# Performance work log

Hardware: AMD Instinct MI355X
Metric: run time of the kernel (lower is better)

The kernel has to match this reference:

```python
import jax, jax.numpy as jnp
import numpy as np

GRID = 16
K = 2
NW = (GRID - K + 1) ** 2  # 225 sliding 2x2 windows on the 16x16 grid


def _make_mask():
    idx = np.arange(GRID * GRID).reshape(GRID, GRID)
    wins = np.stack([idx[i:i + K, j:j + K].ravel()
                     for i in range(GRID - K + 1) for j in range(GRID - K + 1)])
    m = np.zeros((NW, GRID * GRID), np.float32)
    m[np.arange(NW)[:, None], wins] = 1.0
    return jnp.asarray(m)

MASK = _make_mask()          # [225, 256] window -> covered cells
MASK_COUNT = MASK.sum(0)     # windows covering each cell
BN_SCALE = np.float32(1.0 / np.sqrt(1.0 + 1e-5))  # eval BN, running mean=0 var=1


def _adapter(x, w1, w2):
    return jax.nn.relu(jax.nn.relu(x @ w1.T) @ w2.T)


def _bn(x, g, b):
    return x * (g * BN_SCALE) + b


def _head(x, w1, b1, g2, be2, w2, b2, g3, be3, w3, b3):
    x = _bn(jax.nn.relu(x @ w1.T + b1), g2, be2)
    x = _bn(jax.nn.relu(x @ w2.T + b2), g3, be3)
    return jax.nn.sigmoid(x @ w3.T + b3)[:, 0]


def setup_inputs() -> dict:
    B, L, P, D, R, S = 64, 3, 225, 640, 1800, 240
    key = jax.random.key(0)
    ks = jax.random.split(key, 16)
    n = lambda k, s, sc=1.0: jax.random.normal(k, s, jnp.float32) * sc
    te = n(ks[3], (2, D)); te = te / jnp.linalg.norm(te, axis=-1, keepdims=True)
    pr = n(ks[5], (L, R, D)); pr = pr / jnp.linalg.norm(pr, axis=-1, keepdims=True)
    w = 0.05
    return dict(
        image=n(ks[0], (B, 3, S, S)),
        image_embeds=n(ks[1], (B, D)),
        patch_embeds=n(ks[2], (L, B, P, D)),
        text_embeds=te,
        image_embeds_ref=n(ks[4], (1, D)),
        patch_embeds_ref=pr,
        a_w1=n(ks[6], (160, D), w), a_w2=n(ks[7], (D, 160), w),
        r_w1=n(ks[8], (128, D), w), r_b1=jnp.zeros((128,)),
        r_g2=jnp.ones((128,)), r_be2=jnp.zeros((128,)),
        r_w2=n(ks[9], (64, 128), w), r_b2=jnp.zeros((64,)),
        r_g3=jnp.ones((64,)), r_be3=jnp.zeros((64,)),
        r_w3=n(ks[10], (1, 64), w), r_b3=jnp.zeros((1,)),
        h_w1=n(ks[11], (128, P), w), h_b1=jnp.zeros((128,)),
        h_g2=jnp.ones((128,)), h_be2=jnp.zeros((128,)),
        h_w2=n(ks[12], (64, 128), w), h_b2=jnp.zeros((64,)),
        h_g3=jnp.ones((64,)), h_be3=jnp.zeros((64,)),
        h_w3=n(ks[13], (1, 64), w), h_b3=jnp.zeros((1,)),
    )


def reference(image, image_embeds, patch_embeds, text_embeds, image_embeds_ref,
              patch_embeds_ref, a_w1, a_w2,
              r_w1, r_b1, r_g2, r_be2, r_w2, r_b2, r_g3, r_be3, r_w3, r_b3,
              h_w1, h_b1, h_g2, h_be2, h_w2, h_b2, h_g3, h_be3, h_w3, h_b3):
    pe = patch_embeds / jnp.linalg.norm(patch_embeds, axis=-1, keepdims=True)
    nie = image_embeds / jnp.linalg.norm(image_embeds, axis=-1, keepdims=True)
    text_score = jax.nn.softmax(100.0 * nie @ text_embeds.T, axis=-1)[:, 1]
    # kNN-style min-distance over reference patches: [L,B,P,R]
    sim = jnp.einsum('lbpd,lrd->lbpr', pe, patch_embeds_ref)
    patch_ref_map = ((1.0 - sim).min(axis=3) / 2.0).mean(axis=0)  # [B,P]
    fg_score = patch_ref_map.max(axis=1)
    diff = image_embeds_ref - _adapter(image_embeds, a_w1, a_w2)
    img_ref_score = _head(diff, r_w1, r_b1, r_g2, r_be2, r_w2, r_b2, r_g3, r_be3, r_w3, r_b3)
    holistic = (text_score + img_ref_score)[:, None] + patch_ref_map  # [B,225]
    hl_score = _head(holistic, h_w1, h_b1, h_g2, h_be2, h_w2, h_b2, h_g3, h_be3, h_w3, h_b3)
    final_score = (hl_score + fg_score) / 2.0
    # harmonic aggregation of window scores onto the 16x16 grid
    heat = (MASK_COUNT / ((1.0 / holistic) @ MASK)).reshape(-1, GRID, GRID)
    hmap = jax.image.resize(heat, (heat.shape[0], image.shape[2], image.shape[3]), 'bilinear')
    return final_score, hmap
```

## Files before the change

### kernel.cpp

```cpp
#include <hip/hip_runtime.h>
#include <stdint.h>
#include <math.h>

#define L_DIM 3
#define B_DIM 64
#define P_DIM 225
#define D_DIM 640
#define R_DIM 1800
#define S_DIM 240
#define M_TOT 14400
#define M_PAD 14464
#define N_PAD 2048
#define MT 113
#define NT 8
#define KT 20
#define BNSCALE 0.99999500003749981f

typedef __bf16 bf16x8 __attribute__((ext_vector_type(8)));
typedef float f32x4 __attribute__((ext_vector_type(4)));

__device__ __forceinline__ unsigned short f2bf(float f) {
    union { float f; unsigned u; } v; v.f = f;
    unsigned u = v.u;
    unsigned r = (u + 0x7FFFu + ((u >> 16) & 1u)) >> 16;
    return (unsigned short)r;
}

__global__ __launch_bounds__(256)
void k_convert(const float* __restrict__ pe, const float* __restrict__ per,
               unsigned short* __restrict__ abf, unsigned short* __restrict__ rbf,
               float* __restrict__ rnorm)
{
    const int AROWS = L_DIM * M_PAD;
    int wid = (blockIdx.x * 256 + threadIdx.x) >> 6;
    int lane = threadIdx.x & 63;
    const ushort4 z4 = {0, 0, 0, 0};
    if (wid < AROWS) {
        int l = wid / M_PAD, r = wid - l * M_PAD;
        unsigned short* dst = abf + (size_t)wid * D_DIM;
        if (r < M_TOT) {
            const float4* src = (const float4*)(pe + ((size_t)l * M_TOT + r) * D_DIM);
            float ss = 0.f;
            #pragma unroll
            for (int it = 0; it < 3; ++it) {
                int idx = it * 64 + lane;
                if (idx < 160) {
                    float4 v = src[idx];
                    ss += v.x * v.x + v.y * v.y + v.z * v.z + v.w * v.w;
                    ushort4 o;
                    o.x = f2bf(v.x); o.y = f2bf(v.y); o.z = f2bf(v.z); o.w = f2bf(v.w);
                    *(ushort4*)(dst + idx * 4) = o;
                }
            }
            #pragma unroll
            for (int m = 32; m; m >>= 1) ss += __shfl_xor(ss, m);
            if (lane == 0) rnorm[l * M_TOT + r] = rsqrtf(ss);
        } else {
            #pragma unroll
            for (int it = 0; it < 3; ++it) {
                int idx = it * 64 + lane;
                if (idx < 160) *(ushort4*)(dst + idx * 4) = z4;
            }
        }
    } else {
        int w2 = wid - AROWS;
        int l = w2 / N_PAD, r = w2 - l * N_PAD;
        unsigned short* dst = rbf + (size_t)w2 * D_DIM;
        if (r < R_DIM) {
            const float4* src = (const float4*)(per + ((size_t)l * R_DIM + r) * D_DIM);
            #pragma unroll
            for (int it = 0; it < 3; ++it) {
                int idx = it * 64 + lane;
                if (idx < 160) {
                    float4 v = src[idx];
                    ushort4 o;
                    o.x = f2bf(v.x); o.y = f2bf(v.y); o.z = f2bf(v.z); o.w = f2bf(v.w);
                    *(ushort4*)(dst + idx * 4) = o;
                }
            }
        } else {
            #pragma unroll
            for (int it = 0; it < 3; ++it) {
                int idx = it * 64 + lane;
                if (idx < 160) *(ushort4*)(dst + idx * 4) = z4;
            }
        }
    }
}

#define MFMA(A, B, C) __builtin_amdgcn_mfma_f32_16x16x32_bf16((A), (B), (C), 0, 0, 0)
#define GLL(SRC, DSTOFF)                                                     \
    __builtin_amdgcn_global_load_lds(                                        \
        (const __attribute__((address_space(1))) void*)(SRC),               \
        (__attribute__((address_space(3))) void*)(lds + (DSTOFF)), 16, 0, 0)

__global__ __launch_bounds__(512, 4)
void k_gemm_max(const unsigned short* __restrict__ abf,
                const unsigned short* __restrict__ rbf,
                float* __restrict__ pmax)
{
    __shared__ unsigned short lds[36864];
    __shared__ float red[4][128];

    int bid = blockIdx.x;
    int v = (bid & 7) * 339 + (bid >> 3);
    int l = v / (MT * NT);
    int rem = v - l * (MT * NT);
    int mt = rem >> 3;
    int nt = rem & 7;

    int tid = threadIdx.x;
    int wid = tid >> 6, lane = tid & 63;
    int wm = wid >> 2;
    int wn = wid & 3;
    int lane15 = lane & 15, lg = lane >> 4;

    int lpr = lane >> 3;
    int c2  = (lane & 7) ^ lpr;
    int kc  = c2 & 3;
    int rsub = lpr * 2 + (c2 >> 2);
    const unsigned short* gA = abf + (size_t)(l * M_PAD + mt * 128) * D_DIM;
    const unsigned short* gB = rbf + (size_t)(l * N_PAD + nt * 256) * D_DIM;
    const unsigned short* pA  = gA + (size_t)(wid * 16 + rsub) * D_DIM + kc * 8;
    const unsigned short* pB0 = gB + (size_t)(wid * 16 + rsub) * D_DIM + kc * 8;
    const unsigned short* pB1 = gB + (size_t)(wid * 16 + 128 + rsub) * D_DIM + kc * 8;

    int pcom = (((lane15 & 1) << 2) + lg) ^ ((lane15 >> 1) & 7);
    int aoff = (wm * 32 + (lane15 >> 1)) * 64 + pcom * 8;
    int boff = (wn * 32 + (lane15 >> 1)) * 64 + pcom * 8;

    f32x4 acc[4][4];
    #pragma unroll
    for (int mi = 0; mi < 4; ++mi)
        #pragma unroll
        for (int nj = 0; nj < 4; ++nj)
            acc[mi][nj] = f32x4{0.f, 0.f, 0.f, 0.f};

    GLL(pA, wid * 512);
    GLL(pB0, 12288 + wid * 512);
    GLL(pB1, 12288 + (8 + wid) * 512);
    GLL(pA + 32, 4096 + wid * 512);
    GLL(pB0 + 32, 12288 + 8192 + wid * 512);
    GLL(pB1 + 32, 12288 + 8192 + (8 + wid) * 512);
    asm volatile("s_waitcnt vmcnt(3)" ::: "memory");
    __builtin_amdgcn_s_barrier();

    int cur = 0;
    for (int t = 0; t < KT; ++t) {
        int wr = cur + 2; if (wr >= 3) wr -= 3;
        int aB = cur * 4096;
        int bB = 12288 + cur * 8192;

        bf16x8 a[4], b[4];
        #pragma unroll
        for (int mi = 0; mi < 4; ++mi)
            a[mi] = *(const bf16x8*)(lds + aB + aoff + mi * 512);
        #pragma unroll
        for (int nj = 0; nj < 4; ++nj)
            b[nj] = *(const bf16x8*)(lds + bB + boff + nj * 512);

        int koff = (t + 2 < KT ? t + 2 : KT - 1) * 32;
        GLL(pA + koff, wr * 4096 + wid * 512);
        GLL(pB0 + koff, 12288 + wr * 8192 + wid * 512);
        GLL(pB1 + koff, 12288 + wr * 8192 + (8 + wid) * 512);
        asm volatile("s_waitcnt vmcnt(3)" ::: "memory");
        __builtin_amdgcn_s_barrier();

        __builtin_amdgcn_s_setprio(1);
        #pragma unroll
        for (int mi = 0; mi < 4; ++mi)
            #pragma unroll
            for (int nj = 0; nj < 4; ++nj)
                acc[mi][nj] = MFMA(a[mi], b[nj], acc[mi][nj]);
        __builtin_amdgcn_s_setprio(0);

        cur = (cur == 2) ? 0 : cur + 1;
    }

    __syncthreads();

    int colbase = nt * 256 + wn * 64 + lane15;
    #pragma unroll
    for (int mi = 0; mi < 4; ++mi) {
        float t[4] = {-__builtin_inff(), -__builtin_inff(),
                      -__builtin_inff(), -__builtin_inff()};
        #pragma unroll
        for (int nj = 0; nj < 4; ++nj) {
            if (colbase + nj * 16 < R_DIM) {
                #pragma unroll
                for (int r = 0; r < 4; ++r) t[r] = fmaxf(t[r], acc[mi][nj][r]);
            }
        }
        #pragma unroll
        for (int m = 1; m <= 8; m <<= 1) {
            #pragma unroll
            for (int r = 0; r < 4; ++r) t[r] = fmaxf(t[r], __shfl_xor(t[r], m));
        }
        if (lane15 == 0) {
            int rb = wm * 64 + mi * 16 + lg * 4;
            #pragma unroll
            for (int r = 0; r < 4; ++r) red[wn][rb + r] = t[r];
        }
    }
    __syncthreads();
    if (tid < 128) {
        float vmx = fmaxf(fmaxf(red[0][tid], red[1][tid]),
                          fmaxf(red[2][tid], red[3][tid]));
        pmax[((size_t)l * NT + nt) * M_PAD + mt * 128 + tid] = vmx;
    }
}

__device__ __forceinline__ float block_sum8(float v, volatile float* scratch) {
    #pragma unroll
    for (int m = 32; m; m >>= 1) v += __shfl_xor(v, m);
    int w = threadIdx.x >> 6;
    __syncthreads();
    if ((threadIdx.x & 63) == 0) scratch[w] = v;
    __syncthreads();
    float r = 0.f;
    #pragma unroll
    for (int i = 0; i < 8; ++i) r += scratch[i];
    return r;
}
__device__ __forceinline__ float block_max8(float v, volatile float* scratch) {
    #pragma unroll
    for (int m = 32; m; m >>= 1) v = fmaxf(v, __shfl_xor(v, m));
    int w = threadIdx.x >> 6;
    __syncthreads();
    if ((threadIdx.x & 63) == 0) scratch[w] = v;
    __syncthreads();
    float r = scratch[0];
    #pragma unroll
    for (int i = 1; i < 8; ++i) r = fmaxf(r, scratch[i]);
    return r;
}

__global__ __launch_bounds__(512)
void k_small(const float* __restrict__ ie, const float* __restrict__ te,
             const float* __restrict__ ier,
             const float* __restrict__ a_w1, const float* __restrict__ a_w2,
             const float* __restrict__ r_w1, const float* __restrict__ r_b1,
             const float* __restrict__ r_g2, const float* __restrict__ r_be2,
             const float* __restrict__ r_w2, const float* __restrict__ r_b2,
             const float* __restrict__ r_g3, const float* __restrict__ r_be3,
             const float* __restrict__ r_w3, const float* __restrict__ r_b3,
             const float* __restrict__ h_w1, const float* __restrict__ h_b1,
             const float* __restrict__ h_g2, const float* __restrict__ h_be2,
             const float* __restrict__ h_w2, const float* __restrict__ h_b2,
             const float* __restrict__ h_g3, const float* __restrict__ h_be3,
             const float* __restrict__ h_w3, const float* __restrict__ h_b3,
             const float* __restrict__ pmax, const float* __restrict__ rnorm,
             float* __restrict__ out_score, float* __restrict__ outh)
{
    int b = blockIdx.x, tid = threadIdx.x;
    __shared__ float x[D_DIM];
    __shared__ float h1[160];
    __shared__ float dif[D_DIM];
    __shared__ float z1[128];
    __shared__ float z2[64];
    __shared__ float hol[P_DIM];
    __shared__ float rcp[P_DIM];
    __shared__ float heatl[256];
    __shared__ float scratch[8];

    for (int i = tid; i < D_DIM; i += 512) x[i] = ie[b * D_DIM + i];
    __syncthreads();

    float ss = 0.f, d0 = 0.f, d1 = 0.f;
    for (int i = tid; i < D_DIM; i += 512) {
        float v = x[i];
        ss += v * v;
        d0 += v * te[i];
        d1 += v * te[D_DIM + i];
    }
    float ssum = block_sum8(ss, scratch);
    float dd0 = block_sum8(d0, scratch);
    float dd1 = block_sum8(d1, scratch);
    float tscore = 1.f / (1.f + expf(100.f * rsqrtf(ssum) * (dd0 - dd1)));

    for (int o = tid; o < 160; o += 512) {
        const float* w = a_w1 + (size_t)o * D_DIM;
        float s0 = 0, s1 = 0, s2 = 0, s3 = 0;
        for (int d = 0; d < D_DIM; d += 4) {
            s0 += x[d] * w[d]; s1 += x[d + 1] * w[d + 1];
            s2 += x[d + 2] * w[d + 2]; s3 += x[d + 3] * w[d + 3];
        }
        h1[o] = fmaxf((s0 + s1) + (s2 + s3), 0.f);
    }
    __syncthreads();
    for (int d = tid; d < D_DIM; d += 512) {
        const float* w = a_w2 + (size_t)d * 160;
        float s0 = 0, s1 = 0, s2 = 0, s3 = 0;
        for (int o = 0; o < 160; o += 4) {
            s0 += h1[o] * w[o]; s1 += h1[o + 1] * w[o + 1];
            s2 += h1[o + 2] * w[o + 2]; s3 += h1[o + 3] * w[o + 3];
        }
        dif[d] = ier[d] - fmaxf((s0 + s1) + (s2 + s3), 0.f);
    }
    __syncthreads();

    for (int o = tid; o < 128; o += 512) {
        const float* w = r_w1 + (size_t)o * D_DIM;
        float s0 = 0, s1 = 0, s2 = 0, s3 = 0;
        for (int d = 0; d < D_DIM; d += 4) {
            s0 += dif[d] * w[d]; s1 += dif[d + 1] * w[d + 1];
            s2 += dif[d + 2] * w[d + 2]; s3 += dif[d + 3] * w[d + 3];
        }
        float s = (s0 + s1) + (s2 + s3) + r_b1[o];
        z1[o] = fmaxf(s, 0.f) * (r_g2[o] * BNSCALE) + r_be2[o];
    }
    __syncthreads();
    for (int o = tid; o < 64; o += 512) {
        const float* w = r_w2 + (size_t)o * 128;
        float s = r_b2[o];
        for (int d = 0; d < 128; ++d) s += z1[d] * w[d];
        z2[o] = fmaxf(s, 0.f) * (r_g3[o] * BNSCALE) + r_be3[o];
    }
    __syncthreads();
    float sp = (tid < 64) ? z2[tid] * r_w3[tid] : 0.f;
    float irs = 1.f / (1.f + expf(-(block_sum8(sp, scratch) + r_b3[0])));

    float fgp = -__builtin_inff();
    float base = tscore + irs;
    for (int p = tid; p < P_DIM; p += 512) {
        int r = b * P_DIM + p;
        float s = 0.f;
        #pragma unroll
        for (int l = 0; l < L_DIM; ++l) {
            float m = -__builtin_inff();
            #pragma unroll
            for (int t = 0; t < NT; ++t)
                m = fmaxf(m, pmax[((size_t)l * NT + t) * M_PAD + r]);
            s += m * rnorm[l * M_TOT + r];
        }
        float pv = (3.0f - s) / 6.0f;
        fgp = fmaxf(fgp, pv);
        float h = base + pv;
        hol[p] = h;
        rcp[p] = 1.f / h;
    }
    float fg = block_max8(fgp, scratch);

    for (int o = tid; o < 128; o += 512) {
        const float* w = h_w1 + (size_t)o * P_DIM;
        float s = h_b1[o];
        for (int d = 0; d < P_DIM; ++d) s += hol[d] * w[d];
        z1[o] = fmaxf(s, 0.f) * (h_g2[o] * BNSCALE) + h_be2[o];
    }
    __syncthreads();
    for (int o = tid; o < 64; o += 512) {
        const float* w = h_w2 + (size_t)o * 128;
        float s = h_b2[o];
        for (int d = 0; d < 128; ++d) s += z1[d] * w[d];
        z2[o] = fmaxf(s, 0.f) * (h_g3[o] * BNSCALE) + h_be3[o];
    }
    __syncthreads();
    float sp2 = (tid < 64) ? z2[tid] * h_w3[tid] : 0.f;
    float hl_in = block_sum8(sp2, scratch) + h_b3[0];
    if (tid == 0) {
        float hl = 1.f / (1.f + expf(-hl_in));
        out_score[b] = (hl + fg) * 0.5f;
    }

    if (tid < 256) {
        int r = tid >> 4, c = tid & 15;
        float s = 0.f, cnt = 0.f;
        #pragma unroll
        for (int di = -1; di <= 0; ++di) {
            int i = r + di;
            if (i < 0 || i > 14) continue;
            #pragma unroll
            for (int dj = -1; dj <= 0; ++dj) {
                int j = c + dj;
                if (j < 0 || j > 14) continue;
                s += rcp[i * 15 + j];
                cnt += 1.f;
            }
        }
        heatl[tid] = cnt / s;
    }
    __syncthreads();

    float* dst = outh + (size_t)b * (S_DIM * S_DIM);
    for (int px = tid; px < S_DIM * S_DIM; px += 512) {
        int y = px / S_DIM, xc = px - y * S_DIM;
        float sy = fminf(fmaxf((y - 7) * (1.0f / 15.0f), 0.f), 15.f);
        float sx = fminf(fmaxf((xc - 7) * (1.0f / 15.0f), 0.f), 15.f);
        int y0 = (int)sy, x0 = (int)sx;
        int y1 = min(y0 + 1, 15), x1 = min(x0 + 1, 15);
        float fy = sy - (float)y0, fx = sx - (float)x0;
        float v00 = heatl[y0 * 16 + x0], v01 = heatl[y0 * 16 + x1];
        float v10 = heatl[y1 * 16 + x0], v11 = heatl[y1 * 16 + x1];
        float vv = (1.f - fy) * ((1.f - fx) * v00 + fx * v01)
                 + fy * ((1.f - fx) * v10 + fx * v11);
        dst[px] = vv;
    }
}

extern "C" void kernel_launch(void* const* d_in, const int* in_sizes, int n_in,
                              void* d_out, int out_size, void* d_ws, size_t ws_size,
                              hipStream_t stream)
{
    (void)in_sizes; (void)n_in; (void)out_size; (void)ws_size;
    const float* image_embeds = (const float*)d_in[1];
    const float* patch_embeds = (const float*)d_in[2];
    const float* text_embeds  = (const float*)d_in[3];
    const float* ier          = (const float*)d_in[4];
    const float* per          = (const float*)d_in[5];
    const float* a_w1 = (const float*)d_in[6];
    const float* a_w2 = (const float*)d_in[7];
    const float* r_w1 = (const float*)d_in[8];
    const float* r_b1 = (const float*)d_in[9];
    const float* r_g2 = (const float*)d_in[10];
    const float* r_be2 = (const float*)d_in[11];
    const float* r_w2 = (const float*)d_in[12];
    const float* r_b2 = (const float*)d_in[13];
    const float* r_g3 = (const float*)d_in[14];
    const float* r_be3 = (const float*)d_in[15];
    const float* r_w3 = (const float*)d_in[16];
    const float* r_b3 = (const float*)d_in[17];
    const float* h_w1 = (const float*)d_in[18];
    const float* h_b1 = (const float*)d_in[19];
    const float* h_g2 = (const float*)d_in[20];
    const float* h_be2 = (const float*)d_in[21];
    const float* h_w2 = (const float*)d_in[22];
    const float* h_b2 = (const float*)d_in[23];
    const float* h_g3 = (const float*)d_in[24];
    const float* h_be3 = (const float*)d_in[25];
    const float* h_w3 = (const float*)d_in[26];
    const float* h_b3 = (const float*)d_in[27];

    char* ws = (char*)d_ws;
    size_t off = 0;
    auto take = [&](size_t bytes) -> void* {
        void* p = ws + off;
        off += (bytes + 255) & ~(size_t)255;
        return p;
    };
    float* rnorm = (float*)take((size_t)L_DIM * M_TOT * 4);
    float* pmax  = (float*)take((size_t)L_DIM * NT * M_PAD * 4);
    unsigned short* abf = (unsigned short*)take((size_t)L_DIM * M_PAD * D_DIM * 2);
    unsigned short* rbf = (unsigned short*)take((size_t)L_DIM * N_PAD * D_DIM * 2);

    float* out_f = (float*)d_out;

    k_convert<<<dim3((L_DIM * M_PAD + L_DIM * N_PAD) / 4), dim3(256), 0, stream>>>(
        patch_embeds, per, abf, rbf, rnorm);
    k_gemm_max<<<dim3(L_DIM * MT * NT), dim3(512), 0, stream>>>(abf, rbf, pmax);
    k_small<<<dim3(B_DIM), dim3(512), 0, stream>>>(image_embeds, text_embeds, ier,
        a_w1, a_w2, r_w1, r_b1, r_g2, r_be2, r_w2, r_b2, r_g3, r_be3, r_w3, r_b3,
        h_w1, h_b1, h_g2, h_be2, h_w2, h_b2, h_g3, h_be3, h_w3, h_b3,
        pmax, rnorm, out_f, out_f + B_DIM);
}
```

Baseline: 221.8 us.

## Reshape GEMM-max tile to 256x128 with BK=64 double-buffered LDS pipeline

```diff
diff --git a/kernel.cpp b/kernel.cpp
--- a/kernel.cpp
+++ b/kernel.cpp
@@ -9,11 +9,11 @@
 #define R_DIM 1800
 #define S_DIM 240
 #define M_TOT 14400
-#define M_PAD 14464
-#define N_PAD 2048
-#define MT 113
-#define NT 8
-#define KT 20
+#define M_PAD 14592
+#define N_PAD 1920
+#define MT 57
+#define NT 15
+#define KT 10
 #define BNSCALE 0.99999500003749981f
 
 typedef __bf16 bf16x8 __attribute__((ext_vector_type(8)));
@@ -94,40 +94,43 @@
         (const __attribute__((address_space(1))) void*)(SRC),               \
         (__attribute__((address_space(3))) void*)(lds + (DSTOFF)), 16, 0, 0)
 
-__global__ __launch_bounds__(512, 4)
+__global__ __launch_bounds__(512, 1)
 void k_gemm_max(const unsigned short* __restrict__ abf,
                 const unsigned short* __restrict__ rbf,
                 float* __restrict__ pmax)
 {
-    __shared__ unsigned short lds[36864];
-    __shared__ float red[4][128];
+    __shared__ unsigned short lds[49152];
+    __shared__ float red[2][256];
 
     int bid = blockIdx.x;
-    int v = (bid & 7) * 339 + (bid >> 3);
+    int xcd = bid & 7, idx = bid >> 3;
+    int v = (xcd < 5 ? xcd * 321 : 5 * 321 + (xcd - 5) * 320) + idx;
     int l = v / (MT * NT);
     int rem = v - l * (MT * NT);
-    int mt = rem >> 3;
-    int nt = rem & 7;
+    int mt = rem / NT;
+    int nt = rem - mt * NT;
 
     int tid = threadIdx.x;
     int wid = tid >> 6, lane = tid & 63;
-    int wm = wid >> 2;
-    int wn = wid & 3;
+    int wm = wid >> 1;
+    int wn = wid & 1;
     int lane15 = lane & 15, lg = lane >> 4;
-
-    int lpr = lane >> 3;
-    int c2  = (lane & 7) ^ lpr;
-    int kc  = c2 & 3;
-    int rsub = lpr * 2 + (c2 >> 2);
-    const unsigned short* gA = abf + (size_t)(l * M_PAD + mt * 128) * D_DIM;
-    const unsigned short* gB = rbf + (size_t)(l * N_PAD + nt * 256) * D_DIM;
-    const unsigned short* pA  = gA + (size_t)(wid * 16 + rsub) * D_DIM + kc * 8;
-    const unsigned short* pB0 = gB + (size_t)(wid * 16 + rsub) * D_DIM + kc * 8;
-    const unsigned short* pB1 = gB + (size_t)(wid * 16 + 128 + rsub) * D_DIM + kc * 8;
-
-    int pcom = (((lane15 & 1) << 2) + lg) ^ ((lane15 >> 1) & 7);
-    int aoff = (wm * 32 + (lane15 >> 1)) * 64 + pcom * 8;
-    int boff = (wn * 32 + (lane15 >> 1)) * 64 + pcom * 8;
+    int sA = lane15 & 7;
+    int sw0 = (lg ^ sA) << 3;
+    int sw1 = ((4 + lg) ^ sA) << 3;
+    int arow0 = wm * 64 + lane15;
+    int brow0 = wn * 64 + lane15;
+
+    int rowc = lane >> 3;
+    int scol = ((lane & 7) ^ rowc) << 3;
+    const unsigned short* gA = abf + (size_t)(l * M_PAD + mt * 256) * D_DIM;
+    const unsigned short* gB = rbf + (size_t)(l * N_PAD + nt * 128) * D_DIM;
+    const unsigned short* pA0 = gA + (size_t)(wid * 8 + rowc) * D_DIM + scol;
+    const unsigned short* pA1 = gA + (size_t)(64 + wid * 8 + rowc) * D_DIM + scol;
+    const unsigned short* pA2 = gA + (size_t)(128 + wid * 8 + rowc) * D_DIM + scol;
+    const unsigned short* pA3 = gA + (size_t)(192 + wid * 8 + rowc) * D_DIM + scol;
+    const unsigned short* pB0 = gB + (size_t)(wid * 8 + rowc) * D_DIM + scol;
+    const unsigned short* pB1 = gB + (size_t)(64 + wid * 8 + rowc) * D_DIM + scol;
 
     f32x4 acc[4][4];
     #pragma unroll
@@ -136,50 +139,61 @@
         for (int nj = 0; nj < 4; ++nj)
             acc[mi][nj] = f32x4{0.f, 0.f, 0.f, 0.f};
 
-    GLL(pA, wid * 512);
-    GLL(pB0, 12288 + wid * 512);
-    GLL(pB1, 12288 + (8 + wid) * 512);
-    GLL(pA + 32, 4096 + wid * 512);
-    GLL(pB0 + 32, 12288 + 8192 + wid * 512);
-    GLL(pB1 + 32, 12288 + 8192 + (8 + wid) * 512);
-    asm volatile("s_waitcnt vmcnt(3)" ::: "memory");
-    __builtin_amdgcn_s_barrier();
-
-    int cur = 0;
+    GLL(pA0, wid * 512);
+    GLL(pA1, (8 + wid) * 512);
+    GLL(pA2, (16 + wid) * 512);
+    GLL(pA3, (24 + wid) * 512);
+    GLL(pB0, 32768 + wid * 512);
+    GLL(pB1, 32768 + (8 + wid) * 512);
+
+    int buf = 0;
     for (int t = 0; t < KT; ++t) {
-        int wr = cur + 2; if (wr >= 3) wr -= 3;
-        int aB = cur * 4096;
-        int bB = 12288 + cur * 8192;
-
-        bf16x8 a[4], b[4];
-        #pragma unroll
-        for (int mi = 0; mi < 4; ++mi)
-            a[mi] = *(const bf16x8*)(lds + aB + aoff + mi * 512);
-        #pragma unroll
-        for (int nj = 0; nj < 4; ++nj)
-            b[nj] = *(const bf16x8*)(lds + bB + boff + nj * 512);
-
-        int koff = (t + 2 < KT ? t + 2 : KT - 1) * 32;
-        GLL(pA + koff, wr * 4096 + wid * 512);
-        GLL(pB0 + koff, 12288 + wr * 8192 + wid * 512);
-        GLL(pB1 + koff, 12288 + wr * 8192 + (8 + wid) * 512);
-        asm volatile("s_waitcnt vmcnt(3)" ::: "memory");
+        int aB = buf * 16384;
+        int bB = 32768 + buf * 8192;
+
+        asm volatile("s_waitcnt vmcnt(0)" ::: "memory");
         __builtin_amdgcn_s_barrier();
 
+        bf16x8 a[4][2], b[4][2];
+        #pragma unroll
+        for (int mi = 0; mi < 4; ++mi) {
+            a[mi][0] = *(const bf16x8*)(lds + aB + (arow0 + mi * 16) * 64 + sw0);
+            a[mi][1] = *(const bf16x8*)(lds + aB + (arow0 + mi * 16) * 64 + sw1);
+        }
+        #pragma unroll
+        for (int nj = 0; nj < 4; ++nj) {
+            b[nj][0] = *(const bf16x8*)(lds + bB + (brow0 + nj * 16) * 64 + sw0);
+            b[nj][1] = *(const bf16x8*)(lds + bB + (brow0 + nj * 16) * 64 + sw1);
+        }
+
+        if (t + 1 < KT) {
+            int ko = (t + 1) * 64;
+            int oaB = (buf ^ 1) * 16384;
+            int obB = 32768 + (buf ^ 1) * 8192;
+            GLL(pA0 + ko, oaB + wid * 512);
+            GLL(pA1 + ko, oaB + (8 + wid) * 512);
+            GLL(pA2 + ko, oaB + (16 + wid) * 512);
+            GLL(pA3 + ko, oaB + (24 + wid) * 512);
+            GLL(pB0 + ko, obB + wid * 512);
+            GLL(pB1 + ko, obB + (8 + wid) * 512);
+        }
+
         __builtin_amdgcn_s_setprio(1);
         #pragma unroll
-        for (int mi = 0; mi < 4; ++mi)
-            #pragma unroll
-            for (int nj = 0; nj < 4; ++nj)
-                acc[mi][nj] = MFMA(a[mi], b[nj], acc[mi][nj]);
+        for (int ks = 0; ks < 2; ++ks)
+            #pragma unroll
+            for (int mi = 0; mi < 4; ++mi)
+                #pragma unroll
+                for (int nj = 0; nj < 4; ++nj)
+                    acc[mi][nj] = MFMA(a[mi][ks], b[nj][ks], acc[mi][nj]);
         __builtin_amdgcn_s_setprio(0);
 
-        cur = (cur == 2) ? 0 : cur + 1;
-    }
-
-    __syncthreads();
-
-    int colbase = nt * 256 + wn * 64 + lane15;
+        buf ^= 1;
+    }
+
+    __syncthreads();
+
+    int colbase = nt * 128 + wn * 64 + lane15;
     #pragma unroll
     for (int mi = 0; mi < 4; ++mi) {
         float t[4] = {-__builtin_inff(), -__builtin_inff(),
@@ -203,10 +217,9 @@
         }
     }
     __syncthreads();
-    if (tid < 128) {
-        float vmx = fmaxf(fmaxf(red[0][tid], red[1][tid]),
-                          fmaxf(red[2][tid], red[3][tid]));
-        pmax[((size_t)l * NT + nt) * M_PAD + mt * 128 + tid] = vmx;
+    if (tid < 256) {
+        float vmx = fmaxf(red[0][tid], red[1][tid]);
+        pmax[((size_t)l * NT + nt) * M_PAD + mt * 256 + tid] = vmx;
     }
 }
 
```

Measured after the change: 219.7 us. No clear change (-1.0%).

## Enlarge GEMM tile to 256x256 with K=64 double buffering and split resize kernel

Applied to the files above, without the earlier changes.

```diff
diff --git a/kernel.cpp b/kernel.cpp
--- a/kernel.cpp
+++ b/kernel.cpp
@@ -9,11 +9,11 @@
 #define R_DIM 1800
 #define S_DIM 240
 #define M_TOT 14400
-#define M_PAD 14464
+#define M_PAD 14592
 #define N_PAD 2048
-#define MT 113
+#define MT 57
 #define NT 8
-#define KT 20
+#define KT 10
 #define BNSCALE 0.99999500003749981f
 
 typedef __bf16 bf16x8 __attribute__((ext_vector_type(8)));
@@ -93,17 +93,42 @@
     __builtin_amdgcn_global_load_lds(                                        \
         (const __attribute__((address_space(1))) void*)(SRC),               \
         (__attribute__((address_space(3))) void*)(lds + (DSTOFF)), 16, 0, 0)
-
-__global__ __launch_bounds__(512, 4)
+#define BAR() __builtin_amdgcn_s_barrier()
+#define LGKM0() asm volatile("s_waitcnt lgkmcnt(0)" ::: "memory")
+#define VMW(N) asm volatile("s_waitcnt vmcnt(" #N ")" ::: "memory")
+
+#define RDA4(DST, MI0, BASE) do { _Pragma("unroll")                          \
+    for (int mi2 = 0; mi2 < 4; ++mi2) {                                      \
+        DST[mi2][0] = *(const bf16x8*)(lds + (BASE) + (arow + ((MI0)+mi2)*16)*64 + sw0); \
+        DST[mi2][1] = *(const bf16x8*)(lds + (BASE) + (arow + ((MI0)+mi2)*16)*64 + sw1); \
+    } } while (0)
+
+#define RDB2(DST, NJ0, BASE) do { _Pragma("unroll")                          \
+    for (int nj2 = 0; nj2 < 2; ++nj2) {                                      \
+        DST[nj2][0] = *(const bf16x8*)(lds + (BASE) + (brow + ((NJ0)+nj2)*16)*64 + sw0); \
+        DST[nj2][1] = *(const bf16x8*)(lds + (BASE) + (brow + ((NJ0)+nj2)*16)*64 + sw1); \
+    } } while (0)
+
+#define MM8(MI0, NJ0, AFR, BFR) do {                                         \
+    __builtin_amdgcn_s_setprio(1);                                           \
+    _Pragma("unroll") for (int mi2 = 0; mi2 < 4; ++mi2)                      \
+    _Pragma("unroll") for (int nj2 = 0; nj2 < 2; ++nj2)                      \
+    _Pragma("unroll") for (int ks = 0; ks < 2; ++ks)                         \
+        acc[(MI0)+mi2][(NJ0)+nj2] =                                          \
+            MFMA(AFR[mi2][ks], BFR[nj2][ks], acc[(MI0)+mi2][(NJ0)+nj2]);     \
+    __builtin_amdgcn_s_setprio(0);                                           \
+} while (0)
+
+__global__ __launch_bounds__(512, 1)
 void k_gemm_max(const unsigned short* __restrict__ abf,
                 const unsigned short* __restrict__ rbf,
                 float* __restrict__ pmax)
 {
-    __shared__ unsigned short lds[36864];
-    __shared__ float red[4][128];
+    __shared__ unsigned short lds[65536];
+    __shared__ float red[4][256];
 
     int bid = blockIdx.x;
-    int v = (bid & 7) * 339 + (bid >> 3);
+    int v = (bid & 7) * 171 + (bid >> 3);
     int l = v / (MT * NT);
     int rem = v - l * (MT * NT);
     int mt = rem >> 3;
@@ -114,74 +139,96 @@
     int wm = wid >> 2;
     int wn = wid & 3;
     int lane15 = lane & 15, lg = lane >> 4;
-
-    int lpr = lane >> 3;
-    int c2  = (lane & 7) ^ lpr;
-    int kc  = c2 & 3;
-    int rsub = lpr * 2 + (c2 >> 2);
-    const unsigned short* gA = abf + (size_t)(l * M_PAD + mt * 128) * D_DIM;
+    int s7 = lane15 & 7;
+    int sw0 = (lg ^ s7) << 3;
+    int sw1 = ((4 + lg) ^ s7) << 3;
+    int arow = wm * 128 + lane15;
+    int brow = wn * 64 + lane15;
+
+    int rowc = lane >> 3;
+    int scol = ((lane & 7) ^ rowc) << 3;
+    const unsigned short* gA = abf + (size_t)(l * M_PAD + mt * 256) * D_DIM;
     const unsigned short* gB = rbf + (size_t)(l * N_PAD + nt * 256) * D_DIM;
-    const unsigned short* pA  = gA + (size_t)(wid * 16 + rsub) * D_DIM + kc * 8;
-    const unsigned short* pB0 = gB + (size_t)(wid * 16 + rsub) * D_DIM + kc * 8;
-    const unsigned short* pB1 = gB + (size_t)(wid * 16 + 128 + rsub) * D_DIM + kc * 8;
-
-    int pcom = (((lane15 & 1) << 2) + lg) ^ ((lane15 >> 1) & 7);
-    int aoff = (wm * 32 + (lane15 >> 1)) * 64 + pcom * 8;
-    int boff = (wn * 32 + (lane15 >> 1)) * 64 + pcom * 8;
-
-    f32x4 acc[4][4];
-    #pragma unroll
-    for (int mi = 0; mi < 4; ++mi)
+    const unsigned short* sA[2][2];
+    const unsigned short* sB[2][2];
+    int dOf[2][2];
+    #pragma unroll
+    for (int h = 0; h < 2; ++h)
+        #pragma unroll
+        for (int j = 0; j < 2; ++j) {
+            int c = wid * 2 + j;
+            sA[h][j] = gA + (size_t)(h * 128 + c * 8 + rowc) * D_DIM + scol;
+            sB[h][j] = gB + (size_t)(h * 128 + c * 8 + rowc) * D_DIM + scol;
+            dOf[h][j] = h * 8192 + c * 512;
+        }
+
+    f32x4 acc[8][4];
+    #pragma unroll
+    for (int mi = 0; mi < 8; ++mi)
         #pragma unroll
         for (int nj = 0; nj < 4; ++nj)
             acc[mi][nj] = f32x4{0.f, 0.f, 0.f, 0.f};
 
-    GLL(pA, wid * 512);
-    GLL(pB0, 12288 + wid * 512);
-    GLL(pB1, 12288 + (8 + wid) * 512);
-    GLL(pA + 32, 4096 + wid * 512);
-    GLL(pB0 + 32, 12288 + 8192 + wid * 512);
-    GLL(pB1 + 32, 12288 + 8192 + (8 + wid) * 512);
-    asm volatile("s_waitcnt vmcnt(3)" ::: "memory");
-    __builtin_amdgcn_s_barrier();
-
-    int cur = 0;
-    for (int t = 0; t < KT; ++t) {
-        int wr = cur + 2; if (wr >= 3) wr -= 3;
-        int aB = cur * 4096;
-        int bB = 12288 + cur * 8192;
-
-        bf16x8 a[4], b[4];
-        #pragma unroll
-        for (int mi = 0; mi < 4; ++mi)
-            a[mi] = *(const bf16x8*)(lds + aB + aoff + mi * 512);
-        #pragma unroll
-        for (int nj = 0; nj < 4; ++nj)
-            b[nj] = *(const bf16x8*)(lds + bB + boff + nj * 512);
-
-        int koff = (t + 2 < KT ? t + 2 : KT - 1) * 32;
-        GLL(pA + koff, wr * 4096 + wid * 512);
-        GLL(pB0 + koff, 12288 + wr * 8192 + wid * 512);
-        GLL(pB1 + koff, 12288 + wr * 8192 + (8 + wid) * 512);
-        asm volatile("s_waitcnt vmcnt(3)" ::: "memory");
-        __builtin_amdgcn_s_barrier();
-
-        __builtin_amdgcn_s_setprio(1);
-        #pragma unroll
-        for (int mi = 0; mi < 4; ++mi)
-            #pragma unroll
-            for (int nj = 0; nj < 4; ++nj)
-                acc[mi][nj] = MFMA(a[mi], b[nj], acc[mi][nj]);
-        __builtin_amdgcn_s_setprio(0);
-
-        cur = (cur == 2) ? 0 : cur + 1;
+    GLL(sA[0][0], dOf[0][0]);  GLL(sA[0][1], dOf[0][1]);
+    GLL(sA[1][0], dOf[1][0]);  GLL(sA[1][1], dOf[1][1]);
+    GLL(sB[0][0], 32768 + dOf[0][0]);  GLL(sB[0][1], 32768 + dOf[0][1]);
+    GLL(sB[1][0], 32768 + dOf[1][0]);  GLL(sB[1][1], 32768 + dOf[1][1]);
+    GLL(sB[0][0] + 64, 32768 + 16384 + dOf[0][0]);
+    GLL(sB[0][1] + 64, 32768 + 16384 + dOf[0][1]);
+    GLL(sA[0][0] + 64, 16384 + dOf[0][0]);
+    GLL(sA[0][1] + 64, 16384 + dOf[0][1]);
+    VMW(4);
+    BAR();
+
+    for (int T = 0; T < KT; ++T) {
+        int buf = T & 1;
+        int aB = buf * 16384;
+        int bB = 32768 + buf * 16384;
+        int oaB = (buf ^ 1) * 16384;
+        int obB = 32768 + (buf ^ 1) * 16384;
+        int k1 = (T + 1) * 64;
+        int k2 = (T + 2) * 64;
+        bool st1 = (T + 1 < KT);
+        bool st2 = (T + 2 < KT);
+
+        bf16x8 a03[4][2], a47[4][2], b01[2][2], b23[2][2];
+
+        RDA4(a03, 0, aB);
+        RDB2(b01, 0, bB);
+        if (st1) { GLL(sA[1][0] + k1, oaB + dOf[1][0]);
+                   GLL(sA[1][1] + k1, oaB + dOf[1][1]); }
+        BAR(); LGKM0();
+        MM8(0, 0, a03, b01);
+        BAR();
+
+        RDB2(b23, 2, bB);
+        if (st1) { GLL(sB[1][0] + k1, obB + dOf[1][0]);
+                   GLL(sB[1][1] + k1, obB + dOf[1][1]); }
+        BAR(); LGKM0();
+        MM8(0, 2, a03, b23);
+        BAR();
+
+        RDA4(a47, 4, aB);
+        if (st2) { GLL(sB[0][0] + k2, bB + dOf[0][0]);
+                   GLL(sB[0][1] + k2, bB + dOf[0][1]); }
+        BAR(); LGKM0();
+        MM8(4, 0, a47, b01);
+        BAR();
+
+        if (st2) { GLL(sA[0][0] + k2, aB + dOf[0][0]);
+                   GLL(sA[0][1] + k2, aB + dOf[0][1]); }
+        if (T < KT - 2)       { VMW(4); }
+        else if (T == KT - 2) { VMW(0); }
+        BAR();
+        MM8(4, 2, a47, b23);
+        BAR();
     }
 
     __syncthreads();
 
     int colbase = nt * 256 + wn * 64 + lane15;
     #pragma unroll
-    for (int mi = 0; mi < 4; ++mi) {
+    for (int mi = 0; mi < 8; ++mi) {
         float t[4] = {-__builtin_inff(), -__builtin_inff(),
                       -__builtin_inff(), -__builtin_inff()};
         #pragma unroll
@@ -197,16 +244,16 @@
             for (int r = 0; r < 4; ++r) t[r] = fmaxf(t[r], __shfl_xor(t[r], m));
         }
         if (lane15 == 0) {
-            int rb = wm * 64 + mi * 16 + lg * 4;
+            int rb = wm * 128 + mi * 16 + lg * 4;
             #pragma unroll
             for (int r = 0; r < 4; ++r) red[wn][rb + r] = t[r];
         }
     }
     __syncthreads();
-    if (tid < 128) {
+    if (tid < 256) {
         float vmx = fmaxf(fmaxf(red[0][tid], red[1][tid]),
                           fmaxf(red[2][tid], red[3][tid]));
-        pmax[((size_t)l * NT + nt) * M_PAD + mt * 128 + tid] = vmx;
+        pmax[((size_t)l * NT + nt) * M_PAD + mt * 256 + tid] = vmx;
     }
 }
 
@@ -250,7 +297,7 @@
              const float* __restrict__ h_g3, const float* __restrict__ h_be3,
              const float* __restrict__ h_w3, const float* __restrict__ h_b3,
              const float* __restrict__ pmax, const float* __restrict__ rnorm,
-             float* __restrict__ out_score, float* __restrict__ outh)
+             float* __restrict__ heat, float* __restrict__ out_score)
 {
     int b = blockIdx.x, tid = threadIdx.x;
     __shared__ float x[D_DIM];
@@ -260,7 +307,6 @@
     __shared__ float z2[64];
     __shared__ float hol[P_DIM];
     __shared__ float rcp[P_DIM];
-    __shared__ float heatl[256];
     __shared__ float scratch[8];
 
     for (int i = tid; i < D_DIM; i += 512) x[i] = ie[b * D_DIM + i];
@@ -377,23 +423,31 @@
                 cnt += 1.f;
             }
         }
-        heatl[tid] = cnt / s;
-    }
-    __syncthreads();
-
-    float* dst = outh + (size_t)b * (S_DIM * S_DIM);
-    for (int px = tid; px < S_DIM * S_DIM; px += 512) {
+        heat[b * 256 + tid] = cnt / s;
+    }
+}
+
+__global__ __launch_bounds__(256)
+void k_resize(const float* __restrict__ heat, float* __restrict__ outh)
+{
+    int b = blockIdx.x >> 3, sub = blockIdx.x & 7;
+    __shared__ float h[256];
+    if (threadIdx.x < 256) h[threadIdx.x] = heat[b * 256 + threadIdx.x];
+    __syncthreads();
+    int base = sub * 30 * S_DIM;
+    for (int q = threadIdx.x; q < 30 * S_DIM; q += 256) {
+        int px = base + q;
         int y = px / S_DIM, xc = px - y * S_DIM;
         float sy = fminf(fmaxf((y - 7) * (1.0f / 15.0f), 0.f), 15.f);
         float sx = fminf(fmaxf((xc - 7) * (1.0f / 15.0f), 0.f), 15.f);
         int y0 = (int)sy, x0 = (int)sx;
         int y1 = min(y0 + 1, 15), x1 = min(x0 + 1, 15);
         float fy = sy - (float)y0, fx = sx - (float)x0;
-        float v00 = heatl[y0 * 16 + x0], v01 = heatl[y0 * 16 + x1];
-        float v10 = heatl[y1 * 16 + x0], v11 = heatl[y1 * 16 + x1];
-        float vv = (1.f - fy) * ((1.f - fx) * v00 + fx * v01)
-                 + fy * ((1.f - fx) * v10 + fx * v11);
-        dst[px] = vv;
+        float v00 = h[y0 * 16 + x0], v01 = h[y0 * 16 + x1];
+        float v10 = h[y1 * 16 + x0], v11 = h[y1 * 16 + x1];
+        float v = (1.f - fy) * ((1.f - fx) * v00 + fx * v01)
+                + fy * ((1.f - fx) * v10 + fx * v11);
+        outh[(size_t)b * (S_DIM * S_DIM) + px] = v;
     }
 }
 
@@ -439,6 +493,7 @@
     };
     float* rnorm = (float*)take((size_t)L_DIM * M_TOT * 4);
     float* pmax  = (float*)take((size_t)L_DIM * NT * M_PAD * 4);
+    float* heat  = (float*)take((size_t)B_DIM * 256 * 4);
     unsigned short* abf = (unsigned short*)take((size_t)L_DIM * M_PAD * D_DIM * 2);
     unsigned short* rbf = (unsigned short*)take((size_t)L_DIM * N_PAD * D_DIM * 2);
 
@@ -450,5 +505,6 @@
     k_small<<<dim3(B_DIM), dim3(512), 0, stream>>>(image_embeds, text_embeds, ier,
         a_w1, a_w2, r_w1, r_b1, r_g2, r_be2, r_w2, r_b2, r_g3, r_be3, r_w3, r_b3,
         h_w1, h_b1, h_g2, h_be2, h_w2, h_b2, h_g3, h_be3, h_w3, h_b3,
-        pmax, rnorm, out_f, out_f + B_DIM);
-}
+        pmax, rnorm, heat, out_f);
+    k_resize<<<dim3(B_DIM * 8), dim3(256), 0, stream>>>(heat, out_f + B_DIM);
+}
```

Measured after the change: 230.1 us. 3.7% more time.
